# Kernel tuning notes

Hardware: AMD Instinct MI355X
Metric: run time of the kernel (lower is better)

## Reference

```python
import jax, jax.numpy as jnp
import numpy as np

NUM_HEADS = 8
NEG_INF = -1e30


def _within_bucket_rank(idx):
    # idx: [U] int32 bucket ids; returns occurrence count of each id among earlier positions
    U = idx.shape[0]
    order = jnp.argsort(idx, stable=True)
    sv = idx[order]
    pos = jnp.arange(U, dtype=jnp.int32)
    is_start = jnp.concatenate([jnp.ones((1,), bool), sv[1:] != sv[:-1]])
    start = jax.lax.cummax(jnp.where(is_start, pos, 0))
    rank = pos - start
    return jnp.zeros(U, jnp.int32).at[order].set(rank)


def setup_inputs() -> dict:
    key = jax.random.key(0)
    ks = jax.random.split(key, 10)
    B, U, G, E = 8, 16384, 64, 128
    lin = jnp.linspace(0.0, 1.0, G)
    gx, gy = jnp.meshgrid(lin, lin, indexing='ij')
    xc_on_grid = jnp.broadcast_to(jnp.stack([gx, gy], -1), (B, G, G, 2)).astype(jnp.float32)
    s = 0.02
    return {
        'xc_off_grid': jax.random.uniform(ks[0], (B, U, 2), jnp.float32),
        'xc_on_grid': xc_on_grid,
        'zc_off_grid': jax.random.normal(ks[1], (B, U, E), jnp.float32),
        'zc_on_grid': jax.random.normal(ks[2], (B, G, G, E), jnp.float32),
        'latents': jax.random.normal(ks[3], (G * G, E), jnp.float32),
        'fake_embedding': jax.random.normal(ks[4], (E,), jnp.float32),
        'Wq': jax.random.normal(ks[5], (E, E), jnp.float32) * s,
        'Wk': jax.random.normal(ks[6], (E, E), jnp.float32) * s,
        'Wv': jax.random.normal(ks[7], (E, E), jnp.float32) * s,
        'Wo': jax.random.normal(ks[8], (E, E), jnp.float32) * s,
        'ignore_on_grid': 0,
    }


def _bucketize(xc_off_grid, xc_on_grid):
    # returns nearest flat grid index per off-grid point, shape [B, U] int32
    B = xc_off_grid.shape[0]
    dims = xc_on_grid.shape[1:-1]
    S = int(np.prod(dims))
    grid_shape = jnp.asarray(dims, jnp.float32)
    x_on = xc_on_grid.reshape(B, S, -1)
    xmin = x_on.min(axis=(0, 1))
    xmax = x_on.max(axis=(0, 1))
    spacing = (xmax - xmin) / (grid_shape - 1.0)
    nm = jnp.floor((xc_off_grid - xmin + spacing / 2) / spacing)
    nm = jnp.clip(nm, 0.0, grid_shape - 1.0)
    # strides as in the original: flip(cumprod([1, *dims])[:-1])
    strides = np.flip(np.cumprod(np.concatenate([[1], np.asarray(dims)]))[:-1]).astype(np.float32)
    return (nm * jnp.asarray(strides)).sum(-1).astype(jnp.int32)


def _mhca(latents_q, kv, valid, Wq, Wk, Wv, Wo):
    # latents_q: [N,1,E], kv: [N,P,E], valid: [N,P] bool
    N, P, E = kv.shape
    H, Dh = NUM_HEADS, E // NUM_HEADS
    q = (latents_q @ Wq).reshape(N, 1, H, Dh)
    k = (kv @ Wk).reshape(N, P, H, Dh)
    v = (kv @ Wv).reshape(N, P, H, Dh)
    scores = jnp.einsum('nqhd,nkhd->nhqk', q, k) / jnp.sqrt(jnp.asarray(Dh, q.dtype))
    scores = jnp.where(valid[:, None, None, :], scores, NEG_INF)
    attn = jax.nn.softmax(scores, axis=-1)
    out = jnp.einsum('nhqk,nkhd->nqhd', attn, v).reshape(N, 1, E)
    return out @ Wo


def reference(xc_off_grid, xc_on_grid, zc_off_grid, zc_on_grid, latents, fake_embedding, Wq, Wk, Wv, Wo, ignore_on_grid):
    B, U, E = zc_off_grid.shape
    dims = xc_on_grid.shape[1:-1]
    S = int(np.prod(dims))
    z_on = zc_on_grid.reshape(B, S, E)

    nearest_idx = _bucketize(xc_off_grid, xc_on_grid)          # [B, U]
    cumcount = jax.vmap(_within_bucket_rank)(nearest_idx)       # [B, U]
    flat_seg = (nearest_idx + jnp.arange(B, dtype=jnp.int32)[:, None] * S).reshape(-1)
    counts = jax.ops.segment_sum(jnp.ones(B * U, jnp.int32), flat_seg, num_segments=B * S)
    max_patch = int(jax.device_get(counts.max())) + 1           # +1 slot for on-grid/fake token

    # ragged scatter of off-grid tokens into padded per-bucket buffer
    grid_stacked = jnp.zeros((B * S, max_patch, E), zc_off_grid.dtype)
    grid_stacked = grid_stacked.at[flat_seg, cumcount.reshape(-1)].set(zc_off_grid.reshape(B * U, E))
    if ignore_on_grid:
        last = jnp.broadcast_to(fake_embedding, (B * S, E))
    else:
        last = z_on.reshape(B * S, E)
    grid_stacked = grid_stacked.at[:, -1].set(last)

    slot = jnp.arange(max_patch)
    valid = (slot[None, :] < counts[:, None]) | (slot[None, :] == max_patch - 1)  # [B*S, P]

    lat = jnp.broadcast_to(latents[None], (B, S, E)).reshape(B * S, 1, E)
    zc = _mhca(lat, grid_stacked, valid, Wq, Wk, Wv, Wo)        # [B*S, 1, E]
    return zc.reshape(B, *dims, E)
```

## Files before the change

kernel.cpp:

```cpp
#include <hip/hip_runtime.h>
#include <hip/hip_bf16.h>
#include <math.h>

namespace {
constexpr int B_  = 8;
constexpr int U_  = 16384;
constexpr int S_  = 4096;
constexpr int E_  = 128;
constexpr int NTOK  = B_ * U_;
constexpr int NCELL = B_ * S_;
constexpr int CAP = 32;
constexpr int SWZ2 = 2 * 16384;
constexpr int ASZ  = 128 * 1024;
}

typedef __attribute__((ext_vector_type(8))) short bf16x8;
typedef __attribute__((ext_vector_type(4))) float f32x4;

__device__ inline unsigned short bf16rne(float x) {
  unsigned u = __float_as_uint(x);
  u = u + 0x7fffu + ((u >> 16) & 1u);
  return (unsigned short)(u >> 16);
}

__device__ inline float bf16tof(unsigned short h) {
  return __uint_as_float(((unsigned)h) << 16);
}

__device__ inline bf16x8 pack8(float4 a, float4 b) {
  union { __hip_bfloat162 h; unsigned int u; } q0, q1, q2, q3;
  q0.h = __float22bfloat162_rn(make_float2(a.x, a.y));
  q1.h = __float22bfloat162_rn(make_float2(a.z, a.w));
  q2.h = __float22bfloat162_rn(make_float2(b.x, b.y));
  q3.h = __float22bfloat162_rn(make_float2(b.z, b.w));
  union { unsigned int u[4]; bf16x8 v; } r;
  r.u[0] = q0.u; r.u[1] = q1.u; r.u[2] = q2.u; r.u[3] = q3.u;
  return r.v;
}

__global__ __launch_bounds__(1024, 4) void setup_kernel(
    const float* __restrict__ Wq, const float* __restrict__ Wk,
    const float* __restrict__ Wv, const float* __restrict__ Wo,
    const float* __restrict__ xc_off,
    unsigned short* __restrict__ Wsw,
    unsigned short* __restrict__ Ahi, unsigned short* __restrict__ Alo,
    int* __restrict__ cnt, int* __restrict__ sorted) {
  const int tid = threadIdx.x;

  if (blockIdx.x < 16) {
    const int n = tid;
    const int eg = n >> 6, h = (n >> 3) & 7, el = n & 7;
    const int e = eg * 8 + el;
    const float* wk = Wk + (size_t)e * 128 + h * 16;
    float wkv[16];
#pragma unroll
    for (int j = 0; j < 16; j += 4) {
      float4 t = *(const float4*)(wk + j);
      wkv[j] = t.x; wkv[j + 1] = t.y; wkv[j + 2] = t.z; wkv[j + 3] = t.w;
    }
    union { unsigned short s[8]; uint4 v; } rh, rl;
#pragma unroll
    for (int r = 0; r < 8; ++r) {
      const int k = (blockIdx.x << 3) + r;
      const float* wq = Wq + (size_t)k * 128 + h * 16;
      float acc = 0.f;
#pragma unroll
      for (int j = 0; j < 16; j += 4) {
        float4 t = *(const float4*)(wq + j);
        acc = fmaf(t.x, wkv[j], acc);
        acc = fmaf(t.y, wkv[j + 1], acc);
        acc = fmaf(t.z, wkv[j + 2], acc);
        acc = fmaf(t.w, wkv[j + 3], acc);
      }
      acc *= 0.25f;
      const unsigned short hh = bf16rne(acc);
      rh.s[r] = hh;
      rl.s[r] = bf16rne(acc - bf16tof(hh));
    }
    const size_t fo = ((size_t)blockIdx.x * 1024 + n) * 8;
    *(uint4*)(Ahi + fo) = rh.v;
    *(uint4*)(Alo + fo) = rl.v;
  } else {
    const int base = (blockIdx.x - 16) * 1024 + tid;
    const int stride = 112 * 1024;
    for (int i = base; i < SWZ2 + NTOK; i += stride) {
      if (i < SWZ2) {
        const int w = i >> 14, e = i & 16383;
        const int k = e >> 7, n = e & 127;
        const float* src = (w == 0) ? Wv : Wo;
        Wsw[w * 16384 + (((k >> 3) * 128 + n) << 3) + (k & 7)] = bf16rne(src[e]);
      } else {
        const int tok = i - SWZ2;
        const int b = tok >> 14;
        const float sp = 1.0f / 63.0f;
        const float half = sp * 0.5f;
        const float x0 = xc_off[(size_t)tok * 2 + 0];
        const float x1 = xc_off[(size_t)tok * 2 + 1];
        float n0 = floorf((x0 - 0.0f + half) / sp);
        float n1 = floorf((x1 - 0.0f + half) / sp);
        n0 = fminf(fmaxf(n0, 0.0f), 63.0f);
        n1 = fminf(fmaxf(n1, 0.0f), 63.0f);
        const int seg = b * S_ + (int)(n0 * 64.0f + n1);
        const int rank = atomicAdd(&cnt[seg], 1);
        if (rank < CAP) sorted[seg * CAP + rank] = tok;
      }
    }
  }
}

__global__ __launch_bounds__(512, 4) void qkt_gemm(
    const float* __restrict__ latents,
    const unsigned short* __restrict__ Ahi,
    const unsigned short* __restrict__ Alo,
    unsigned short* __restrict__ QKt) {
  const int tid = threadIdx.x;
  const int wave = tid >> 6, lane = tid & 63;
  const int c = lane & 15, g = lane >> 4;
  const int rb = blockIdx.x >> 1, cb = blockIdx.x & 1;
  const int wr = wave >> 2, wc = wave & 3;
  const int t0 = rb * 32 + wr * 16;
  const int n0 = cb * 512 + wc * 128;

  f32x4 acc[8];
#pragma unroll
  for (int i = 0; i < 8; ++i) acc[i] = {0.f, 0.f, 0.f, 0.f};

  const float* arow = latents + (size_t)(t0 + c) * E_ + g * 8;
#pragma unroll
  for (int ks = 0; ks < 4; ++ks) {
    float4 a0 = *(const float4*)(arow + ks * 32);
    float4 a1 = *(const float4*)(arow + ks * 32 + 4);
    bf16x8 af = pack8(a0, a1);
    const size_t kg = (size_t)(ks * 4 + g) * 1024;
#pragma unroll
    for (int nt = 0; nt < 8; ++nt) {
      const size_t fo = (kg + n0 + nt * 16 + c) * 8;
      acc[nt] = __builtin_amdgcn_mfma_f32_16x16x32_bf16(
          af, *(const bf16x8*)(Ahi + fo), acc[nt], 0, 0, 0);
      acc[nt] = __builtin_amdgcn_mfma_f32_16x16x32_bf16(
          af, *(const bf16x8*)(Alo + fo), acc[nt], 0, 0, 0);
    }
  }
#pragma unroll
  for (int nt = 0; nt < 8; ++nt)
#pragma unroll
    for (int r = 0; r < 4; ++r)
      QKt[(size_t)(t0 + g * 4 + r) * 1024 + n0 + nt * 16 + c] = bf16rne(acc[nt][r]);
}

__global__ __launch_bounds__(512, 4) void fused_cells(
    const float* __restrict__ zc_off, const float* __restrict__ zc_on,
    const float* __restrict__ fake, const int* __restrict__ ignore_flag,
    const unsigned short* __restrict__ Wv_sw,
    const unsigned short* __restrict__ QKt, const int* __restrict__ cnt,
    const int* __restrict__ sorted, float* __restrict__ out) {
  __shared__ __align__(16) unsigned short wv[16384];
  __shared__ float wbuf[8][16][9];
  const int tid = threadIdx.x;
  {
    const uint4* sv = (const uint4*)Wv_sw;
    uint4* dv = (uint4*)wv;
#pragma unroll
    for (int i = 0; i < 4; ++i) dv[i * 512 + tid] = sv[i * 512 + tid];
  }
  const int ign = *ignore_flag;
  __syncthreads();

  const int wave = tid >> 6, lane = tid & 63;
  const int c = lane & 15, g = lane >> 4;
  const int half = c >> 3;
  const int hwr  = g >> 1;
  const bf16x8* bv = (const bf16x8*)wv;

  const int slot = blockIdx.x * 8 + wave;
  const int cA = slot * 2, cB = cA + 1;
  const int sA = cA & (S_ - 1);
  const int nA = min(cnt[cA], CAP);
  const int nB = min(cnt[cB], CAP);
  const int cH = half ? cB : cA;
  const int nH = half ? nB : nA;
  const int baseH = cH * CAP;
  const bf16x8* bqk = (const bf16x8*)(QKt + (size_t)(sA + half) * 1024);

  float num_acc[8], den_acc[8];
#pragma unroll
  for (int i = 0; i < 8; ++i) { num_acc[i] = 0.f; den_acc[i] = 0.f; }

  const int chunks = max((nA + 8) >> 3, (nB + 8) >> 3);

  for (int ch = 0; ch < chunks; ++ch) {
    const int jj = ch * 8 + (c & 7);
    const float* arow;
    if (jj < nH)       arow = zc_off + (size_t)sorted[baseH + jj] * E_;
    else if (jj == nH) arow = ign ? fake : (zc_on + (size_t)cH * E_);
    else               arow = zc_on;
    arow += g * 8;

    bf16x8 af[4];
#pragma unroll
    for (int ks = 0; ks < 4; ++ks) {
      float4 a0 = *(const float4*)(arow + ks * 32);
      float4 a1 = *(const float4*)(arow + ks * 32 + 4);
      af[ks] = pack8(a0, a1);
    }

    f32x4 aS = {0.f, 0.f, 0.f, 0.f};
#pragma unroll
    for (int ks = 0; ks < 4; ++ks)
      aS = __builtin_amdgcn_mfma_f32_16x16x32_bf16(af[ks], bqk[(ks * 4 + g) * 8 + (c & 7)], aS, 0, 0, 0);

    if (hwr == half) {
#pragma unroll
      for (int r = 0; r < 4; ++r) {
        const int t = g * 4 + r;
        const int jt = ch * 8 + (t & 7);
        wbuf[wave][t][c & 7] = (jt <= nH) ? __expf(aS[r]) : 0.f;
      }
    }

#pragma unroll 2
    for (int h = 0; h < 8; ++h) {
      float wr[4];
#pragma unroll
      for (int r = 0; r < 4; ++r) wr[r] = wbuf[wave][g * 4 + r][h];

      const int bo = g * 128 + c + h * 16;
      f32x4 aV = {0.f, 0.f, 0.f, 0.f};
#pragma unroll
      for (int ks = 0; ks < 4; ++ks)
        aV = __builtin_amdgcn_mfma_f32_16x16x32_bf16(af[ks], bv[bo + ks * 512], aV, 0, 0, 0);

      float sv = 0.f, sd = 0.f;
#pragma unroll
      for (int r = 0; r < 4; ++r) { sv = fmaf(wr[r], aV[r], sv); sd += wr[r]; }
      num_acc[h] += sv;
      den_acc[h] += sd;
    }
  }

#pragma unroll
  for (int i = 0; i < 8; ++i) {
    num_acc[i] += __shfl_xor(num_acc[i], 16, 64);
    den_acc[i] += __shfl_xor(den_acc[i], 16, 64);
  }
  const int cellO = hwr ? cB : cA;
  const int hb = (g & 1) * 4;
#pragma unroll
  for (int b = 0; b < 4; ++b) {
    const int h = hb + b;
    out[(size_t)cellO * E_ + h * 16 + c] = num_acc[h] / den_acc[h];
  }
}

__global__ __launch_bounds__(512, 4) void finalize_mfma(
    const unsigned short* __restrict__ Wo_sw, float* __restrict__ out) {
  __shared__ __align__(16) unsigned short wo[16384];
  const int tid = threadIdx.x;
  {
    const uint4* s = (const uint4*)Wo_sw;
    uint4* d = (uint4*)wo;
#pragma unroll
    for (int i = 0; i < 4; ++i) d[i * 512 + tid] = s[i * 512 + tid];
  }
  __syncthreads();

  const int wave = tid >> 6, lane = tid & 63;
  const int c = lane & 15, g = lane >> 4;
  const int t0w = blockIdx.x * 128 + wave * 16;

  f32x4 acc[8];
#pragma unroll
  for (int i = 0; i < 8; ++i) acc[i] = {0.f, 0.f, 0.f, 0.f};

  const float* nrow = out + (size_t)(t0w + c) * E_ + g * 8;
  const bf16x8* bo_ = (const bf16x8*)wo;
#pragma unroll
  for (int ks = 0; ks < 4; ++ks) {
    float4 a0 = *(const float4*)(nrow + ks * 32);
    float4 a1 = *(const float4*)(nrow + ks * 32 + 4);
    bf16x8 af = pack8(a0, a1);
    const int bofs = (ks * 4 + g) * 128 + c;
#pragma unroll
    for (int nt = 0; nt < 8; ++nt)
      acc[nt] = __builtin_amdgcn_mfma_f32_16x16x32_bf16(af, bo_[bofs + nt * 16], acc[nt], 0, 0, 0);
  }
#pragma unroll
  for (int nt = 0; nt < 8; ++nt)
#pragma unroll
    for (int r = 0; r < 4; ++r)
      out[(size_t)(t0w + g * 4 + r) * E_ + nt * 16 + c] = acc[nt][r];
}

extern "C" void kernel_launch(void* const* d_in, const int* in_sizes, int n_in,
                              void* d_out, int out_size, void* d_ws, size_t ws_size,
                              hipStream_t stream) {
  const float* xc_off  = (const float*)d_in[0];
  const float* zc_off  = (const float*)d_in[2];
  const float* zc_on   = (const float*)d_in[3];
  const float* latents = (const float*)d_in[4];
  const float* fake    = (const float*)d_in[5];
  const float* Wq      = (const float*)d_in[6];
  const float* Wk      = (const float*)d_in[7];
  const float* Wv      = (const float*)d_in[8];
  const float* Wo      = (const float*)d_in[9];
  const int*   ignore  = (const int*)d_in[10];

  float* out = (float*)d_out;

  unsigned short* QKt = (unsigned short*)d_ws;
  unsigned short* Wsw = QKt + (size_t)S_ * 1024;
  int* cnt    = (int*)(Wsw + SWZ2);
  int* sorted = cnt + NCELL;
  unsigned short* Ahi = (unsigned short*)(sorted + NCELL * CAP);
  unsigned short* Alo = Ahi + ASZ;
  unsigned short* Wv_sw = Wsw;
  unsigned short* Wo_sw = Wsw + 16384;

  hipMemsetAsync(cnt, 0, NCELL * sizeof(int), stream);
  setup_kernel<<<128, 1024, 0, stream>>>(Wq, Wk, Wv, Wo, xc_off,
                                         Wsw, Ahi, Alo, cnt, sorted);
  qkt_gemm<<<256, 512, 0, stream>>>(latents, Ahi, Alo, QKt);
  fused_cells<<<2048, 512, 0, stream>>>(zc_off, zc_on, fake, ignore,
                                        Wv_sw, QKt, cnt, sorted, out);
  finalize_mfma<<<NCELL / 128, 512, 0, stream>>>(Wo_sw, out);
}
```

Baseline: 191.4 us.

## Fuse output projection into cell attention kernel via shared-memory staging

Removes the separate finalize_mfma launch and performs the Wo projection at the end of fused_cells. Per-cell attention outputs are staged in reused shared memory (the Wv buffer), and each wave computes one 16-column slice of the 16-cell × 128 output with Wo fragments loaded straight from global memory. This avoids writing intermediate results to global memory, reading them back, and paying one extra kernel launch. The cost is an extra block barrier and per-block Wo fragment loads from global/L2.

```diff
diff --git a/kernel.cpp b/kernel.cpp
--- a/kernel.cpp
+++ b/kernel.cpp
@@ -152,6 +152,7 @@
     const float* __restrict__ zc_off, const float* __restrict__ zc_on,
     const float* __restrict__ fake, const int* __restrict__ ignore_flag,
     const unsigned short* __restrict__ Wv_sw,
+    const unsigned short* __restrict__ Wo_sw,
     const unsigned short* __restrict__ QKt, const int* __restrict__ cnt,
     const int* __restrict__ sorted, float* __restrict__ out) {
   __shared__ __align__(16) unsigned short wv[16384];
@@ -243,52 +244,36 @@
     num_acc[i] += __shfl_xor(num_acc[i], 16, 64);
     den_acc[i] += __shfl_xor(den_acc[i], 16, 64);
   }
-  const int cellO = hwr ? cB : cA;
   const int hb = (g & 1) * 4;
+
+  bf16x8 wof[4];
+#pragma unroll
+  for (int ks = 0; ks < 4; ++ks)
+    wof[ks] = *(const bf16x8*)(Wo_sw +
+        ((size_t)((ks * 4 + g) * 128 + wave * 16 + c)) * 8);
+
+  __syncthreads();
+  float* obuf = (float*)wv;
+  const int lrow = wave * 2 + hwr;
 #pragma unroll
   for (int b = 0; b < 4; ++b) {
     const int h = hb + b;
-    out[(size_t)cellO * E_ + h * 16 + c] = num_acc[h] / den_acc[h];
-  }
-}
-
-__global__ __launch_bounds__(512, 4) void finalize_mfma(
-    const unsigned short* __restrict__ Wo_sw, float* __restrict__ out) {
-  __shared__ __align__(16) unsigned short wo[16384];
-  const int tid = threadIdx.x;
-  {
-    const uint4* s = (const uint4*)Wo_sw;
-    uint4* d = (uint4*)wo;
-#pragma unroll
-    for (int i = 0; i < 4; ++i) d[i * 512 + tid] = s[i * 512 + tid];
+    obuf[lrow * 132 + h * 16 + c] = num_acc[h] / den_acc[h];
   }
   __syncthreads();
 
-  const int wave = tid >> 6, lane = tid & 63;
-  const int c = lane & 15, g = lane >> 4;
-  const int t0w = blockIdx.x * 128 + wave * 16;
-
-  f32x4 acc[8];
-#pragma unroll
-  for (int i = 0; i < 8; ++i) acc[i] = {0.f, 0.f, 0.f, 0.f};
-
-  const float* nrow = out + (size_t)(t0w + c) * E_ + g * 8;
-  const bf16x8* bo_ = (const bf16x8*)wo;
+  const float* nrow = obuf + c * 132 + g * 8;
+  f32x4 acc2 = {0.f, 0.f, 0.f, 0.f};
 #pragma unroll
   for (int ks = 0; ks < 4; ++ks) {
     float4 a0 = *(const float4*)(nrow + ks * 32);
     float4 a1 = *(const float4*)(nrow + ks * 32 + 4);
-    bf16x8 af = pack8(a0, a1);
-    const int bofs = (ks * 4 + g) * 128 + c;
-#pragma unroll
-    for (int nt = 0; nt < 8; ++nt)
-      acc[nt] = __builtin_amdgcn_mfma_f32_16x16x32_bf16(af, bo_[bofs + nt * 16], acc[nt], 0, 0, 0);
-  }
-#pragma unroll
-  for (int nt = 0; nt < 8; ++nt)
-#pragma unroll
-    for (int r = 0; r < 4; ++r)
-      out[(size_t)(t0w + g * 4 + r) * E_ + nt * 16 + c] = acc[nt][r];
+    acc2 = __builtin_amdgcn_mfma_f32_16x16x32_bf16(pack8(a0, a1), wof[ks], acc2, 0, 0, 0);
+  }
+  const int cell0 = blockIdx.x * 16;
+#pragma unroll
+  for (int r = 0; r < 4; ++r)
+    out[(size_t)(cell0 + g * 4 + r) * E_ + wave * 16 + c] = acc2[r];
 }
 
 extern "C" void kernel_launch(void* const* d_in, const int* in_sizes, int n_in,
@@ -321,6 +306,5 @@
                                          Wsw, Ahi, Alo, cnt, sorted);
   qkt_gemm<<<256, 512, 0, stream>>>(latents, Ahi, Alo, QKt);
   fused_cells<<<2048, 512, 0, stream>>>(zc_off, zc_on, fake, ignore,
-                                        Wv_sw, QKt, cnt, sorted, out);
-  finalize_mfma<<<NCELL / 128, 512, 0, stream>>>(Wo_sw, out);
-}
+                                        Wv_sw, Wo_sw, QKt, cnt, sorted, out);
+}
```

After: 188.7 us. Within noise of the previous version (-1.4%).
